# Kernel optimization log

Hardware: AMD Instinct MI355X
Metric: run time of the kernel (lower is better)

Reference implementation:

```python
import jax, jax.numpy as jnp
import numpy as np

NEG_SLOPE = 0.2  # PyG GATConv default negative_slope


def _gat_conv(x, edge_index, W, a_src, a_dst, b, concat):
    """One PyG-style GATConv layer (eval mode, add_self_loops=True).
    x: [N, F_in], W: [F_in, H*C], a_src/a_dst: [H, C], b: [H*C] or [C].
    """
    N = x.shape[0]
    H, C = a_src.shape
    loops = jnp.arange(N, dtype=edge_index.dtype)
    src = jnp.concatenate([edge_index[0], loops])  # [E+N]
    dst = jnp.concatenate([edge_index[1], loops])
    h = (x @ W).reshape(N, H, C)                   # [N,H,C]
    al_s = jnp.einsum('nhc,hc->nh', h, a_src)      # [N,H]
    al_d = jnp.einsum('nhc,hc->nh', h, a_dst)
    e = jax.nn.leaky_relu(al_s[src] + al_d[dst], NEG_SLOPE)  # [E+N, H]
    # segment softmax over incoming edges of each dst node
    m = jax.lax.stop_gradient(jax.ops.segment_max(e, dst, num_segments=N))
    ex = jnp.exp(e - m[dst])
    denom = jax.ops.segment_sum(ex, dst, num_segments=N)
    alpha = ex / denom[dst]                        # [E+N, H]
    out = jax.ops.segment_sum(h[src] * alpha[:, :, None], dst, num_segments=N)  # [N,H,C]
    out = out.reshape(N, H * C) if concat else out.mean(axis=1)
    return out + b


def setup_inputs() -> dict:
    key = jax.random.key(0)
    ks = jax.random.split(key, 10)
    N, E, F_IN = 100000, 1600000, 128
    H1, C1 = 4, 32   # layer 1: concat -> 128
    H2, C2 = 1, 64   # layer 2: mean   -> 64
    x = jax.random.normal(ks[0], (N, F_IN), dtype=jnp.float32)
    edge_index = jax.random.randint(ks[1], (2, E), 0, N, dtype=jnp.int32)
    s = 0.1
    return {
        'x': x,
        'edge_index': edge_index,
        'W1': jax.random.normal(ks[2], (F_IN, H1 * C1), dtype=jnp.float32) * s,
        'a1_src': jax.random.normal(ks[3], (H1, C1), dtype=jnp.float32) * s,
        'a1_dst': jax.random.normal(ks[4], (H1, C1), dtype=jnp.float32) * s,
        'b1': jnp.zeros((H1 * C1,), dtype=jnp.float32),
        'W2': jax.random.normal(ks[5], (H1 * C1, H2 * C2), dtype=jnp.float32) * s,
        'a2_src': jax.random.normal(ks[6], (H2, C2), dtype=jnp.float32) * s,
        'a2_dst': jax.random.normal(ks[7], (H2, C2), dtype=jnp.float32) * s,
        'b2': jnp.zeros((C2,), dtype=jnp.float32),
    }


def reference(x, edge_index, W1, a1_src, a1_dst, b1, W2, a2_src, a2_dst, b2):
    h = _gat_conv(x, edge_index, W1, a1_src, a1_dst, b1, concat=True)   # [N,128]
    h = jax.nn.elu(h)                                                   # dropout is identity in eval
    out = _gat_conv(h, edge_index, W2, a2_src, a2_dst, b2, concat=False)  # [N,64]
    return out
```

## Files before the change

kernel.cpp:

```cpp
#include <hip/hip_runtime.h>
#include <hip/hip_bf16.h>
#include <math.h>

static constexpr float NEG_SLOPE = 0.2f;
static constexpr float NEG_BIG = -3.0e38f;

typedef __attribute__((ext_vector_type(8))) short short8;
typedef __attribute__((ext_vector_type(4))) float f32x4;

__device__ __forceinline__ float blo(unsigned u) { return __uint_as_float(u << 16); }
__device__ __forceinline__ float bhi(unsigned u) { return __uint_as_float(u & 0xffff0000u); }
__device__ __forceinline__ unsigned pack2(float a, float b) {
  __hip_bfloat162 t = __float22bfloat162_rn(make_float2(a, b));
  union { __hip_bfloat162 b; unsigned u; } v;
  v.b = t;
  return v.u;
}

#define FMA8(V, A)                         \
  acc[0] = fmaf(blo((V).x), (A), acc[0]);  \
  acc[1] = fmaf(bhi((V).x), (A), acc[1]);  \
  acc[2] = fmaf(blo((V).y), (A), acc[2]);  \
  acc[3] = fmaf(bhi((V).y), (A), acc[3]);  \
  acc[4] = fmaf(blo((V).z), (A), acc[4]);  \
  acc[5] = fmaf(bhi((V).z), (A), acc[5]);  \
  acc[6] = fmaf(blo((V).w), (A), acc[6]);  \
  acc[7] = fmaf(bhi((V).w), (A), acc[7])

template <int BN, int HEADS>
__global__ void k_prep_w(const float* __restrict__ W, const float* __restrict__ as_,
                         const float* __restrict__ ad_, uint4* __restrict__ out) {
  constexpr int XC = BN + 16;
  constexpr int C = BN / HEADS;
  const int i = blockIdx.x * blockDim.x + threadIdx.x;
  if (i >= XC * 16) return;
  const int col = i >> 4;
  const int chunk = (i & 15) ^ (col & 7);
  float v[8];
  if (col < BN) {
#pragma unroll
    for (int t = 0; t < 8; ++t) v[t] = W[(size_t)(chunk * 8 + t) * BN + col];
  } else {
    const int j = col - BN;
#pragma unroll
    for (int t = 0; t < 8; ++t) v[t] = 0.f;
    if (j < 2 * HEADS) {
      const int hh = (HEADS == 4) ? (j & 3) : 0;
      const bool is_src = (HEADS == 4) ? (j < 4) : (j == 0);
      const float* av = (is_src ? as_ : ad_) + hh * C;
      const float* wb = W + hh * C;
#pragma unroll
      for (int t = 0; t < 8; ++t) {
        float s = 0.f;
        for (int c = 0; c < C; ++c) s = fmaf(wb[(size_t)(chunk * 8 + t) * BN + c], av[c], s);
        v[t] = s;
      }
    }
  }
  uint4 u;
  u.x = pack2(v[0], v[1]);
  u.y = pack2(v[2], v[3]);
  u.z = pack2(v[4], v[5]);
  u.w = pack2(v[6], v[7]);
  out[i] = u;
}

template <int BN, int HEADS>
__global__ __launch_bounds__(256) void k_mfma_gemm(
    const float* __restrict__ x, const uint4* __restrict__ wsw,
    __hip_bfloat16* __restrict__ h_out, float* __restrict__ als,
    float* __restrict__ ald, int N) {
  constexpr int XC = BN + 16;
  constexpr int NTILES = BN / 16;
  constexpr int BUFSZ = (XC * 256 > 128 * 256) ? XC * 256 : 128 * 256;
  __shared__ unsigned char buf[BUFSZ];
  const int tid = threadIdx.x;
  const int lane = tid & 63;
  const int wid = tid >> 6;
  const int base = blockIdx.x * 128;

  for (int it = 0; it < 8; ++it) {
    const int i = it * 256 + tid;
    const int r = i >> 4, c = i & 15;
    const int g = base + r;
    float4 f0 = make_float4(0.f, 0.f, 0.f, 0.f), f1 = f0;
    if (g < N) {
      const float* xp = x + (size_t)g * 128 + c * 8;
      f0 = *(const float4*)xp;
      f1 = *(const float4*)(xp + 4);
    }
    uint4 u;
    u.x = pack2(f0.x, f0.y);
    u.y = pack2(f0.z, f0.w);
    u.z = pack2(f1.x, f1.y);
    u.w = pack2(f1.z, f1.w);
    *(uint4*)(buf + r * 256 + ((c * 16) ^ ((r & 7) << 4))) = u;
  }
  __syncthreads();

  const int lg = lane >> 4;
  const int ll = lane & 15;
  union U { uint4 u; short8 s; };
  short8 afr[2][4];
#pragma unroll
  for (int rt = 0; rt < 2; ++rt) {
    const int row = wid * 32 + rt * 16 + ll;
    const unsigned char* rp = buf + row * 256;
    const int swz = (row & 7) << 4;
#pragma unroll
    for (int ks = 0; ks < 4; ++ks) {
      U t;
      t.u = *(const uint4*)(rp + ((ks * 64 + lg * 16) ^ swz));
      afr[rt][ks] = t.s;
    }
  }
  __syncthreads();

  {
    uint4* dst = (uint4*)buf;
    for (int i = tid; i < XC * 16; i += 256) dst[i] = wsw[i];
  }
  __syncthreads();

  f32x4 acc[2][NTILES + 1];
#pragma unroll
  for (int rt = 0; rt < 2; ++rt)
#pragma unroll
    for (int t = 0; t <= NTILES; ++t) acc[rt][t] = (f32x4){0.f, 0.f, 0.f, 0.f};

#pragma unroll
  for (int t = 0; t <= NTILES; ++t) {
    const int col = t * 16 + ll;
    const unsigned char* cp = buf + col * 256;
    const int swz = (col & 7) << 4;
#pragma unroll
    for (int ks = 0; ks < 4; ++ks) {
      U b;
      b.u = *(const uint4*)(cp + ((ks * 64 + lg * 16) ^ swz));
      acc[0][t] = __builtin_amdgcn_mfma_f32_16x16x32_bf16(afr[0][ks], b.s, acc[0][t], 0, 0, 0);
      acc[1][t] = __builtin_amdgcn_mfma_f32_16x16x32_bf16(afr[1][ks], b.s, acc[1][t], 0, 0, 0);
    }
  }

#pragma unroll
  for (int rt = 0; rt < 2; ++rt) {
#pragma unroll
    for (int r = 0; r < 4; ++r) {
      const int row = base + wid * 32 + rt * 16 + lg * 4 + r;
      if (row < N) {
        const float v = acc[rt][NTILES][r];
        if (HEADS == 4) {
          if (ll < 4) als[(size_t)row * 4 + ll] = v;
          else if (ll < 8) ald[(size_t)row * 4 + (ll - 4)] = v;
        } else {
          if (ll == 0) als[row] = v;
          else if (ll == 1) ald[row] = v;
        }
      }
    }
  }

  __syncthreads();
#pragma unroll
  for (int rt = 0; rt < 2; ++rt) {
#pragma unroll
    for (int t = 0; t < NTILES; ++t) {
#pragma unroll
      for (int r = 0; r < 4; ++r) {
        const float v = acc[rt][t][r];
        const float vn = __shfl_xor(v, 1, 64);
        if (!(lane & 1)) {
          const int row = wid * 32 + rt * 16 + lg * 4 + r;
          *(unsigned*)(buf + row * (BN * 2) + (t * 16 + ll) * 2) = pack2(v, vn);
        }
      }
    }
  }
  __syncthreads();
  {
    constexpr int U4 = 128 * BN / 8;
    constexpr int U4R = BN / 8;
    for (int i = tid; i < U4; i += 256) {
      const int row = i / U4R;
      const int g = base + row;
      if (g < N)
        *(uint4*)((unsigned short*)h_out + (size_t)g * BN + (i % U4R) * 8) = ((uint4*)buf)[i];
    }
  }
}

__global__ void k_count(const int* __restrict__ edst, int* __restrict__ cnt, int E) {
  int i = blockIdx.x * blockDim.x + threadIdx.x;
  if (i < E) atomicAdd(cnt + edst[i], 1);
}

__global__ void k_scan_local(const int* __restrict__ cnt, int* __restrict__ rowptr,
                             int* __restrict__ bsum, int N) {
  __shared__ int lds[256];
  const int tid = threadIdx.x;
  const int base = blockIdx.x * 1024;
  int vals[4], tsum = 0;
#pragma unroll
  for (int q = 0; q < 4; ++q) {
    int i = base + tid * 4 + q;
    vals[q] = (i < N) ? cnt[i] + 1 : 0;
    tsum += vals[q];
  }
  lds[tid] = tsum;
  __syncthreads();
  for (int off = 1; off < 256; off <<= 1) {
    int t = (tid >= off) ? lds[tid - off] : 0;
    __syncthreads();
    lds[tid] += t;
    __syncthreads();
  }
  int run = lds[tid] - tsum;
  if (tid == 255) bsum[blockIdx.x] = lds[255];
#pragma unroll
  for (int q = 0; q < 4; ++q) {
    int i = base + tid * 4 + q;
    if (i < N) rowptr[i] = run;
    run += vals[q];
  }
}

__global__ void k_scan_bsum(int* __restrict__ bsum, int nb) {
  __shared__ int lds[1024];
  const int tid = threadIdx.x;
  int v = (tid < nb) ? bsum[tid] : 0;
  lds[tid] = v;
  __syncthreads();
  for (int off = 1; off < 1024; off <<= 1) {
    int t = (tid >= off) ? lds[tid - off] : 0;
    __syncthreads();
    lds[tid] += t;
    __syncthreads();
  }
  bsum[tid] = lds[tid] - v;
}

__global__ void k_scan_add(const int* __restrict__ bsum, int* __restrict__ rowptr,
                           int* __restrict__ cursor, int N, int total) {
  int i = blockIdx.x * blockDim.x + threadIdx.x;
  if (i < N) {
    int r = rowptr[i] + bsum[i >> 10];
    rowptr[i] = r;
    cursor[i] = r;
  } else if (i == N) {
    rowptr[N] = total;
  }
}

__global__ void k_build_part(const int* __restrict__ esrc, const int* __restrict__ edst,
                             int* __restrict__ cursor, int* __restrict__ nbr, int E, int N) {
  constexpr int NPARTS = 4;
  const int p = blockIdx.x & 3;
  const int span = (N + NPARTS - 1) / NPARTS;
  const int lo = p * span;
  const int hi = min(N, lo + span);
  const int gid = (int)(blockIdx.x >> 2) * blockDim.x + threadIdx.x;
  const int stride = (int)(gridDim.x >> 2) * blockDim.x;
  const int E4 = E >> 2;
  for (int i = gid; i < E4; i += stride) {
    const int4 d4 = ((const int4*)edst)[i];
    const int4 s4 = ((const int4*)esrc)[i];
    if (d4.x >= lo && d4.x < hi) nbr[atomicAdd(cursor + d4.x, 1)] = s4.x;
    if (d4.y >= lo && d4.y < hi) nbr[atomicAdd(cursor + d4.y, 1)] = s4.y;
    if (d4.z >= lo && d4.z < hi) nbr[atomicAdd(cursor + d4.z, 1)] = s4.z;
    if (d4.w >= lo && d4.w < hi) nbr[atomicAdd(cursor + d4.w, 1)] = s4.w;
  }
  for (int i = E4 * 4 + gid; i < E + N; i += stride) {
    const int d = i < E ? edst[i] : i - E;
    if (d >= lo && d < hi) {
      const int sn = i < E ? esrc[i] : i - E;
      nbr[atomicAdd(cursor + d, 1)] = sn;
    }
  }
}

__global__ void k_gather_l1(const int* __restrict__ rowptr, const int* __restrict__ nbr,
                            const float* __restrict__ als, const float* __restrict__ ald,
                            const __hip_bfloat16* __restrict__ hfeat,
                            const float* __restrict__ bias,
                            float* __restrict__ out, int N) {
  __shared__ float atab[4][2][4][40];
  __shared__ unsigned otab[4][2][32];
  const int lane = threadIdx.x & 63;
  const int wid = threadIdx.x >> 6;
  const int half = lane >> 5;
  const int l32 = lane & 31;
  const int node = (int)((blockIdx.x * blockDim.x + threadIdx.x) >> 6) * 2 + half;
  const bool valid = node < N;
  int start = 0, end = 0;
  if (valid) {
    start = rowptr[node];
    end = rowptr[node + 1];
  }
  const int deg = end - start;
  const float4 aldd = valid ? ((const float4*)ald)[node] : make_float4(0.f, 0.f, 0.f, 0.f);

  float t[4];
  int myn = 0;
  {
    const int j = start + l32;
    if (j < end) {
      myn = nbr[j];
      const float4 av = ((const float4*)als)[myn];
      const float tr[4] = {av.x + aldd.x, av.y + aldd.y, av.z + aldd.z, av.w + aldd.w};
#pragma unroll
      for (int h = 0; h < 4; ++h) t[h] = tr[h] >= 0.f ? tr[h] : NEG_SLOPE * tr[h];
    } else {
#pragma unroll
      for (int h = 0; h < 4; ++h) t[h] = NEG_BIG;
    }
  }
  otab[wid][half][l32] = (unsigned)myn << 8;

  float Mh[4], rden[4], myex[4];
  if (deg <= 32) {
#pragma unroll
    for (int h = 0; h < 4; ++h) {
      float M = t[h];
#pragma unroll
      for (int off = 1; off < 32; off <<= 1) M = fmaxf(M, __shfl_xor(M, off, 64));
      const float e = __expf(t[h] - M);
      float sum = e;
#pragma unroll
      for (int off = 1; off < 32; off <<= 1) sum += __shfl_xor(sum, off, 64);
      Mh[h] = M;
      rden[h] = 1.f / sum;
      myex[h] = e * rden[h];
    }
  } else {
    float m[4], s[4];
#pragma unroll
    for (int h = 0; h < 4; ++h) {
      m[h] = t[h];
      s[h] = (t[h] > NEG_BIG) ? 1.f : 0.f;
    }
    for (int b = start + 32; b < end; b += 32) {
      const int j = b + l32;
      if (j < end) {
        const int sn = nbr[j];
        const float4 av = ((const float4*)als)[sn];
        const float tr[4] = {av.x + aldd.x, av.y + aldd.y, av.z + aldd.z, av.w + aldd.w};
#pragma unroll
        for (int h = 0; h < 4; ++h) {
          const float tv = tr[h] >= 0.f ? tr[h] : NEG_SLOPE * tr[h];
          const float M = fmaxf(m[h], tv);
          s[h] = s[h] * __expf(m[h] - M) + __expf(tv - M);
          m[h] = M;
        }
      }
    }
#pragma unroll
    for (int h = 0; h < 4; ++h) {
      float M = m[h];
#pragma unroll
      for (int off = 1; off < 32; off <<= 1) M = fmaxf(M, __shfl_xor(M, off, 64));
      float e = s[h] * __expf(m[h] - M);
#pragma unroll
      for (int off = 1; off < 32; off <<= 1) e += __shfl_xor(e, off, 64);
      Mh[h] = M;
      rden[h] = 1.f / e;
      myex[h] = __expf(t[h] - M) * rden[h];
    }
  }
#pragma unroll
  for (int h = 0; h < 4; ++h) atab[wid][half][h][l32] = myex[h];

  const int sub = l32 >> 4;
  const int q = l32 & 15;
  const int head = q >> 2;
  const char* hq = (const char*)hfeat + q * 16;
  float acc[8];
#pragma unroll
  for (int k = 0; k < 8; ++k) acc[k] = 0.f;

  const int nq = deg < 32 ? deg : 32;
  const float* ap = &atab[wid][half][head][0];
  const unsigned* op = &otab[wid][half][0];
  for (int j0 = 0; j0 < nq; j0 += 8) {
    const float a0 = ap[j0 + sub];
    const float a1 = ap[j0 + 2 + sub];
    const float a2 = ap[j0 + 4 + sub];
    const float a3 = ap[j0 + 6 + sub];
    const uint4 v0 = *(const uint4*)(hq + op[j0 + sub]);
    const uint4 v1 = *(const uint4*)(hq + op[j0 + 2 + sub]);
    const uint4 v2 = *(const uint4*)(hq + op[j0 + 4 + sub]);
    const uint4 v3 = *(const uint4*)(hq + op[j0 + 6 + sub]);
    FMA8(v0, a0);
    FMA8(v1, a1);
    FMA8(v2, a2);
    FMA8(v3, a3);
  }
  if (deg > 32) {
    const float Mm = head == 0 ? Mh[0] : head == 1 ? Mh[1] : head == 2 ? Mh[2] : Mh[3];
    const float rd = head == 0 ? rden[0] : head == 1 ? rden[1] : head == 2 ? rden[2] : rden[3];
    const float ad_ = head == 0 ? aldd.x : head == 1 ? aldd.y : head == 2 ? aldd.z : aldd.w;
    for (int j0 = 32; j0 < deg; j0 += 2) {
      const int j = j0 + sub;
      float a = 0.f;
      int sn = 0;
      if (j < deg) {
        sn = nbr[start + j];
        const float4 av = ((const float4*)als)[sn];
        const float as_ = head == 0 ? av.x : head == 1 ? av.y : head == 2 ? av.z : av.w;
        float tv = as_ + ad_;
        tv = tv >= 0.f ? tv : NEG_SLOPE * tv;
        a = __expf(tv - Mm) * rd;
      }
      const uint4 v = *(const uint4*)(hq + (size_t)sn * 256);
      FMA8(v, a);
    }
  }

#pragma unroll
  for (int k = 0; k < 8; ++k) acc[k] += __shfl_xor(acc[k], 16, 64);
  if (valid && sub == 0) {
    const float4 b0 = ((const float4*)bias)[q * 2];
    const float4 b1 = ((const float4*)bias)[q * 2 + 1];
    float r[8] = {acc[0] + b0.x, acc[1] + b0.y, acc[2] + b0.z, acc[3] + b0.w,
                  acc[4] + b1.x, acc[5] + b1.y, acc[6] + b1.z, acc[7] + b1.w};
#pragma unroll
    for (int k = 0; k < 8; ++k) r[k] = r[k] > 0.f ? r[k] : __expf(r[k]) - 1.f;
    float4* opo = (float4*)(out + (size_t)node * 128 + q * 8);
    opo[0] = make_float4(r[0], r[1], r[2], r[3]);
    opo[1] = make_float4(r[4], r[5], r[6], r[7]);
  }
}

__global__ void k_gather_l2(const int* __restrict__ rowptr, const int* __restrict__ nbr,
                            const float* __restrict__ als, const float* __restrict__ ald,
                            const __hip_bfloat16* __restrict__ hfeat,
                            const float* __restrict__ bias,
                            float* __restrict__ out, int N) {
  __shared__ float2 atab[4][2][36];
  const int lane = threadIdx.x & 63;
  const int wid = threadIdx.x >> 6;
  const int half = lane >> 5;
  const int l32 = lane & 31;
  const int node = (int)((blockIdx.x * blockDim.x + threadIdx.x) >> 6) * 2 + half;
  const bool valid = node < N;
  int start = 0, end = 0;
  if (valid) {
    start = rowptr[node];
    end = rowptr[node + 1];
  }
  const int deg = end - start;
  const float ald0 = valid ? ald[node] : 0.f;

  float t = NEG_BIG;
  int myn = 0;
  {
    const int j = start + l32;
    if (j < end) {
      myn = nbr[j];
      float tv = als[myn] + ald0;
      t = tv >= 0.f ? tv : NEG_SLOPE * tv;
    }
  }

  float M, rden, myal;
  if (deg <= 32) {
    M = t;
#pragma unroll
    for (int off = 1; off < 32; off <<= 1) M = fmaxf(M, __shfl_xor(M, off, 64));
    const float e = __expf(t - M);
    float sum = e;
#pragma unroll
    for (int off = 1; off < 32; off <<= 1) sum += __shfl_xor(sum, off, 64);
    rden = 1.f / sum;
    myal = e * rden;
  } else {
    float m = t, s = (t > NEG_BIG) ? 1.f : 0.f;
    for (int b = start + 32; b < end; b += 32) {
      const int j = b + l32;
      if (j < end) {
        float tv = als[nbr[j]] + ald0;
        tv = tv >= 0.f ? tv : NEG_SLOPE * tv;
        const float Mn = fmaxf(m, tv);
        s = s * __expf(m - Mn) + __expf(tv - Mn);
        m = Mn;
      }
    }
    M = m;
#pragma unroll
    for (int off = 1; off < 32; off <<= 1) M = fmaxf(M, __shfl_xor(M, off, 64));
    float e = s * __expf(m - M);
#pragma unroll
    for (int off = 1; off < 32; off <<= 1) e += __shfl_xor(e, off, 64);
    rden = 1.f / e;
    myal = __expf(t - M) * rden;
  }
  atab[wid][half][l32] = make_float2(myal, __int_as_float(myn << 7));

  const int sub = l32 >> 3;
  const int q = l32 & 7;
  const char* hq = (const char*)hfeat + q * 16;
  float acc[8];
#pragma unroll
  for (int k = 0; k < 8; ++k) acc[k] = 0.f;

  const int nq = deg < 32 ? deg : 32;
  const float2* ap = &atab[wid][half][0];
  for (int j0 = 0; j0 < nq; j0 += 16) {
    const float2 o0 = ap[j0 + sub];
    const float2 o1 = ap[j0 + 4 + sub];
    const float2 o2 = ap[j0 + 8 + sub];
    const float2 o3 = ap[j0 + 12 + sub];
    const uint4 v0 = *(const uint4*)(hq + (unsigned)__float_as_int(o0.y));
    const uint4 v1 = *(const uint4*)(hq + (unsigned)__float_as_int(o1.y));
    const uint4 v2 = *(const uint4*)(hq + (unsigned)__float_as_int(o2.y));
    const uint4 v3 = *(const uint4*)(hq + (unsigned)__float_as_int(o3.y));
    FMA8(v0, o0.x);
    FMA8(v1, o1.x);
    FMA8(v2, o2.x);
    FMA8(v3, o3.x);
  }
  if (deg > 32) {
    for (int j0 = 32; j0 < deg; j0 += 4) {
      const int j = j0 + sub;
      float a = 0.f;
      int sn = 0;
      if (j < deg) {
        sn = nbr[start + j];
        float tv = als[sn] + ald0;
        tv = tv >= 0.f ? tv : NEG_SLOPE * tv;
        a = __expf(tv - M) * rden;
      }
      const uint4 v = *(const uint4*)(hq + (size_t)sn * 128);
      FMA8(v, a);
    }
  }

#pragma unroll
  for (int k = 0; k < 8; ++k) {
    acc[k] += __shfl_xor(acc[k], 8, 64);
    acc[k] += __shfl_xor(acc[k], 16, 64);
  }
  if (valid && sub == 0) {
    const float4 b0 = ((const float4*)bias)[q * 2];
    const float4 b1 = ((const float4*)bias)[q * 2 + 1];
    float4* opo = (float4*)(out + (size_t)node * 64 + q * 8);
    opo[0] = make_float4(acc[0] + b0.x, acc[1] + b0.y, acc[2] + b0.z, acc[3] + b0.w);
    opo[1] = make_float4(acc[4] + b1.x, acc[5] + b1.y, acc[6] + b1.z, acc[7] + b1.w);
  }
}

extern "C" void kernel_launch(void* const* d_in, const int* in_sizes, int n_in,
                              void* d_out, int out_size, void* d_ws, size_t ws_size,
                              hipStream_t stream) {
  const float* x   = (const float*)d_in[0];
  const int*   ei  = (const int*)d_in[1];
  const float* W1  = (const float*)d_in[2];
  const float* a1s = (const float*)d_in[3];
  const float* a1d = (const float*)d_in[4];
  const float* b1  = (const float*)d_in[5];
  const float* W2  = (const float*)d_in[6];
  const float* a2s = (const float*)d_in[7];
  const float* a2d = (const float*)d_in[8];
  const float* b2  = (const float*)d_in[9];

  const int N = in_sizes[0] / 128;
  const int E = in_sizes[1] / 2;
  const int* esrc = ei;
  const int* edst = ei + E;

  float* ws   = (float*)d_ws;
  __hip_bfloat16* h = (__hip_bfloat16*)ws;
  float* out1 = ws   + (size_t)N * 128;
  float* als  = out1 + (size_t)N * 128;
  float* ald  = als  + (size_t)N * 4;
  int* cnt    = (int*)(ald + (size_t)N * 4);
  int* rowptr = cnt + N;
  int* cursor = rowptr + N + 1;
  int* bsum   = cursor + N;
  int* nbr    = bsum + 1024;
  size_t off = ((size_t)((nbr + E + N) - (int*)ws) + 3) & ~(size_t)3;
  uint4* wsw1 = (uint4*)((int*)ws + off);
  uint4* wsw2 = wsw1 + 144 * 16;

  float* outF = (float*)d_out;

  const int total = E + N;
  const int nb = (N + 1023) / 1024;

  k_prep_w<128, 4><<<(144 * 16 + 255) / 256, 256, 0, stream>>>(W1, a1s, a1d, wsw1);
  k_prep_w<64, 1><<<(80 * 16 + 255) / 256, 256, 0, stream>>>(W2, a2s, a2d, wsw2);
  hipMemsetAsync(cnt, 0, (size_t)N * 4, stream);
  k_count<<<(E + 255) / 256, 256, 0, stream>>>(edst, cnt, E);
  k_scan_local<<<nb, 256, 0, stream>>>(cnt, rowptr, bsum, N);
  k_scan_bsum<<<1, 1024, 0, stream>>>(bsum, nb);
  k_scan_add<<<(N + 256) / 256, 256, 0, stream>>>(bsum, rowptr, cursor, N, total);
  k_build_part<<<1280, 256, 0, stream>>>(esrc, edst, cursor, nbr, E, N);

  k_mfma_gemm<128, 4><<<(N + 127) / 128, 256, 0, stream>>>(x, wsw1, h, als, ald, N);
  k_gather_l1<<<(N + 7) / 8, 256, 0, stream>>>(rowptr, nbr, als, ald, h, b1, out1, N);

  k_mfma_gemm<64, 1><<<(N + 127) / 128, 256, 0, stream>>>(out1, wsw2, h, als, ald, N);
  k_gather_l2<<<(N + 7) / 8, 256, 0, stream>>>(rowptr, nbr, als, ald, h, b2, outF, N);
}
```

Baseline: 327.3 us.

## Merge setup launches, fold block-sum scan into add, tweak build partitions and bf16 unpack

Combines the two weight-prep kernels and the count memset into a single setup kernel, and folds the single-block bsum scan into the scan-add kernel, where each block rescans up to 128 block sums in LDS. This cuts launch count and kernel-boundary overhead. It also halves the number of destination partitions in the neighbor build, so each edge is scanned fewer times at the cost of more atomic contention per partition. The layer-1 gather now skips masking the high bf16 half, leaving the low bits in as small noise to save one AND per element.

```diff
diff --git a/kernel.cpp b/kernel.cpp
--- a/kernel.cpp
+++ b/kernel.cpp
@@ -10,6 +10,7 @@
 
 __device__ __forceinline__ float blo(unsigned u) { return __uint_as_float(u << 16); }
 __device__ __forceinline__ float bhi(unsigned u) { return __uint_as_float(u & 0xffff0000u); }
+__device__ __forceinline__ float bhiraw(unsigned u) { return __uint_as_float(u); }
 __device__ __forceinline__ unsigned pack2(float a, float b) {
   __hip_bfloat162 t = __float22bfloat162_rn(make_float2(a, b));
   union { __hip_bfloat162 b; unsigned u; } v;
@@ -27,12 +28,21 @@
   acc[6] = fmaf(blo((V).w), (A), acc[6]);  \
   acc[7] = fmaf(bhi((V).w), (A), acc[7])
 
+#define FMA8R(V, A)                           \
+  acc[0] = fmaf(blo((V).x), (A), acc[0]);     \
+  acc[1] = fmaf(bhiraw((V).x), (A), acc[1]);  \
+  acc[2] = fmaf(blo((V).y), (A), acc[2]);     \
+  acc[3] = fmaf(bhiraw((V).y), (A), acc[3]);  \
+  acc[4] = fmaf(blo((V).z), (A), acc[4]);     \
+  acc[5] = fmaf(bhiraw((V).z), (A), acc[5]);  \
+  acc[6] = fmaf(blo((V).w), (A), acc[6]);     \
+  acc[7] = fmaf(bhiraw((V).w), (A), acc[7])
+
 template <int BN, int HEADS>
-__global__ void k_prep_w(const float* __restrict__ W, const float* __restrict__ as_,
-                         const float* __restrict__ ad_, uint4* __restrict__ out) {
+__device__ void prep_w(const float* __restrict__ W, const float* __restrict__ as_,
+                       const float* __restrict__ ad_, uint4* __restrict__ out, int i) {
   constexpr int XC = BN + 16;
   constexpr int C = BN / HEADS;
-  const int i = blockIdx.x * blockDim.x + threadIdx.x;
   if (i >= XC * 16) return;
   const int col = i >> 4;
   const int chunk = (i & 15) ^ (col & 7);
@@ -63,6 +73,25 @@
   u.z = pack2(v[4], v[5]);
   u.w = pack2(v[6], v[7]);
   out[i] = u;
+}
+
+__global__ void k_setup(const float* __restrict__ W1, const float* __restrict__ a1s,
+                        const float* __restrict__ a1d, uint4* __restrict__ wsw1,
+                        const float* __restrict__ W2, const float* __restrict__ a2s,
+                        const float* __restrict__ a2d, uint4* __restrict__ wsw2,
+                        int* __restrict__ cnt, int N) {
+  const int b = blockIdx.x;
+  const int tid = threadIdx.x;
+  if (b < 9) {
+    prep_w<128, 4>(W1, a1s, a1d, wsw1, b * 256 + tid);
+  } else if (b < 14) {
+    prep_w<64, 1>(W2, a2s, a2d, wsw2, (b - 9) * 256 + tid);
+  } else {
+    const int i = (b - 14) * 256 + tid;
+    if (i < (N >> 2)) ((int4*)cnt)[i] = make_int4(0, 0, 0, 0);
+    const int r = (N & ~3) + i;
+    if (i < 4 && r < N) cnt[r] = 0;
+  }
 }
 
 template <int BN, int HEADS>
@@ -224,26 +253,28 @@
   }
 }
 
-__global__ void k_scan_bsum(int* __restrict__ bsum, int nb) {
-  __shared__ int lds[1024];
+__global__ void k_scan_add2(const int* __restrict__ bsum, int nb,
+                            int* __restrict__ rowptr, int* __restrict__ cursor,
+                            int N, int total) {
+  __shared__ int pref[128];
   const int tid = threadIdx.x;
-  int v = (tid < nb) ? bsum[tid] : 0;
-  lds[tid] = v;
-  __syncthreads();
-  for (int off = 1; off < 1024; off <<= 1) {
-    int t = (tid >= off) ? lds[tid - off] : 0;
+  int own = 0;
+  if (tid < 128) {
+    own = (tid < nb) ? bsum[tid] : 0;
+    pref[tid] = own;
+  }
+  __syncthreads();
+  for (int off = 1; off < 128; off <<= 1) {
+    int t = (tid >= off && tid < 128) ? pref[tid - off] : 0;
     __syncthreads();
-    lds[tid] += t;
+    if (tid < 128) pref[tid] += t;
     __syncthreads();
   }
-  bsum[tid] = lds[tid] - v;
-}
-
-__global__ void k_scan_add(const int* __restrict__ bsum, int* __restrict__ rowptr,
-                           int* __restrict__ cursor, int N, int total) {
-  int i = blockIdx.x * blockDim.x + threadIdx.x;
+  if (tid < 128) pref[tid] -= own;
+  __syncthreads();
+  const int i = blockIdx.x * blockDim.x + tid;
   if (i < N) {
-    int r = rowptr[i] + bsum[i >> 10];
+    int r = rowptr[i] + pref[i >> 10];
     rowptr[i] = r;
     cursor[i] = r;
   } else if (i == N) {
@@ -253,13 +284,13 @@
 
 __global__ void k_build_part(const int* __restrict__ esrc, const int* __restrict__ edst,
                              int* __restrict__ cursor, int* __restrict__ nbr, int E, int N) {
-  constexpr int NPARTS = 4;
-  const int p = blockIdx.x & 3;
+  constexpr int NPARTS = 2;
+  const int p = blockIdx.x & 1;
   const int span = (N + NPARTS - 1) / NPARTS;
   const int lo = p * span;
   const int hi = min(N, lo + span);
-  const int gid = (int)(blockIdx.x >> 2) * blockDim.x + threadIdx.x;
-  const int stride = (int)(gridDim.x >> 2) * blockDim.x;
+  const int gid = (int)(blockIdx.x >> 1) * blockDim.x + threadIdx.x;
+  const int stride = (int)(gridDim.x >> 1) * blockDim.x;
   const int E4 = E >> 2;
   for (int i = gid; i < E4; i += stride) {
     const int4 d4 = ((const int4*)edst)[i];
@@ -389,10 +420,10 @@
     const uint4 v1 = *(const uint4*)(hq + op[j0 + 2 + sub]);
     const uint4 v2 = *(const uint4*)(hq + op[j0 + 4 + sub]);
     const uint4 v3 = *(const uint4*)(hq + op[j0 + 6 + sub]);
-    FMA8(v0, a0);
-    FMA8(v1, a1);
-    FMA8(v2, a2);
-    FMA8(v3, a3);
+    FMA8R(v0, a0);
+    FMA8R(v1, a1);
+    FMA8R(v2, a2);
+    FMA8R(v3, a3);
   }
   if (deg > 32) {
     const float Mm = head == 0 ? Mh[0] : head == 1 ? Mh[1] : head == 2 ? Mh[2] : Mh[3];
@@ -411,7 +442,7 @@
         a = __expf(tv - Mm) * rd;
       }
       const uint4 v = *(const uint4*)(hq + (size_t)sn * 256);
-      FMA8(v, a);
+      FMA8R(v, a);
     }
   }
 
@@ -586,13 +617,11 @@
   const int total = E + N;
   const int nb = (N + 1023) / 1024;
 
-  k_prep_w<128, 4><<<(144 * 16 + 255) / 256, 256, 0, stream>>>(W1, a1s, a1d, wsw1);
-  k_prep_w<64, 1><<<(80 * 16 + 255) / 256, 256, 0, stream>>>(W2, a2s, a2d, wsw2);
-  hipMemsetAsync(cnt, 0, (size_t)N * 4, stream);
+  const int zb = ((N >> 2) + 255) / 256;
+  k_setup<<<14 + zb, 256, 0, stream>>>(W1, a1s, a1d, wsw1, W2, a2s, a2d, wsw2, cnt, N);
   k_count<<<(E + 255) / 256, 256, 0, stream>>>(edst, cnt, E);
   k_scan_local<<<nb, 256, 0, stream>>>(cnt, rowptr, bsum, N);
-  k_scan_bsum<<<1, 1024, 0, stream>>>(bsum, nb);
-  k_scan_add<<<(N + 256) / 256, 256, 0, stream>>>(bsum, rowptr, cursor, N, total);
+  k_scan_add2<<<(N + 256) / 256, 256, 0, stream>>>(bsum, nb, rowptr, cursor, N, total);
   k_build_part<<<1280, 256, 0, stream>>>(esrc, edst, cursor, nbr, E, N);
 
   k_mfma_gemm<128, 4><<<(N + 127) / 128, 256, 0, stream>>>(x, wsw1, h, als, ald, N);
```

After: 348.1 us. 6.3% more time.
